# Optimization experiments

Measured on AMD Instinct MI355X. Metric: run time of the kernel, lower is better.

The kernel has to match this reference:

```python
import jax, jax.numpy as jnp
import numpy as np

B, S, D = 1, 1024, 4096
N_HEADS, N_KV, HEAD_DIM = 32, 8, 128
ALPHA = 5.0
BUDGET = 0.2
NEG = -10000.0


def rotate_half(x):
    x1 = x[..., : x.shape[-1] // 2]
    x2 = x[..., x.shape[-1] // 2 :]
    return jnp.concatenate((-x2, x1), axis=-1)


def kv_cache_mask(scores):
    # scores: [b, h, T, S]. Faithful vectorized version of the torch per-row
    # topk/scatter loop (capacity=1.0 => eviction loop body never executes).
    b, h, T, Ssrc = scores.shape
    attn = scores.reshape(b * h, T, Ssrc)
    causal_add = jnp.triu(jnp.full((T, Ssrc), NEG, scores.dtype), 1)
    attn = attn + causal_add
    # torch: torch.max(attn, -1, keepdim=True)[0][0] -> row maxes of head 0 only
    max_val = jnp.max(attn[0], axis=-1, keepdims=True)  # [T, 1]
    fetch_num = jnp.sum(attn >= (max_val - ALPHA), axis=-1)  # [BH, T]
    fetch_num = jnp.mean(fetch_num.astype(scores.dtype), axis=0).astype(jnp.int32)  # [T]
    fetch_max = int(Ssrc * BUDGET)
    fetch_num = jnp.minimum(fetch_num, fetch_max)
    # rank of every column within its (row-causal-masked) row, descending score
    order = jnp.argsort(-attn, axis=-1)           # [BH, T, S]
    ranks = jnp.argsort(order, axis=-1)           # [BH, T, S]
    rows = jnp.arange(T)
    keep_topk = ranks < fetch_num[None, :, None]  # variable-k topk per row
    tril = jnp.arange(Ssrc)[None, :] <= rows[:, None]  # dense causal rows
    fetch = jnp.where((rows < fetch_max)[None, :, None], tril[None], keep_topk)
    mask = jnp.where(fetch, 0.0, NEG).astype(scores.dtype).reshape(b, h, T, Ssrc)
    density = fetch.astype(jnp.float32).sum() / (b * h) / (T * (T + 1) / 2)
    return mask, density


def setup_inputs() -> dict:
    key = jax.random.key(0)
    ks = jax.random.split(key, 5)
    hidden_states = jax.random.normal(ks[0], (B, S, D), jnp.float32)
    # standard RoPE tables, theta=10000
    inv_freq = 1.0 / (10000.0 ** (np.arange(0, HEAD_DIM, 2, dtype=np.float64) / HEAD_DIM))
    freqs = np.outer(np.arange(S, dtype=np.float64), inv_freq)  # [S, hd/2]
    emb = np.concatenate([freqs, freqs], axis=-1)               # [S, hd]
    cos = jnp.asarray(np.cos(emb), jnp.float32)[None]           # [1, S, hd]
    sin = jnp.asarray(np.sin(emb), jnp.float32)[None]
    Wq = jax.random.normal(ks[1], (N_HEADS * HEAD_DIM, D), jnp.float32) * 0.02
    Wk = jax.random.normal(ks[2], (N_KV * HEAD_DIM, D), jnp.float32) * 0.02
    Wv = jax.random.normal(ks[3], (N_KV * HEAD_DIM, D), jnp.float32) * 0.02
    Wo = jax.random.normal(ks[4], (D, N_HEADS * HEAD_DIM), jnp.float32) * 0.02
    return {"hidden_states": hidden_states, "cos": cos, "sin": sin,
            "Wq": Wq, "Wk": Wk, "Wv": Wv, "Wo": Wo}


def reference(hidden_states, cos, sin, Wq, Wk, Wv, Wo):
    b, s, d = hidden_states.shape
    scaling = HEAD_DIM ** -0.5
    q = (hidden_states @ Wq.T).reshape(b, s, N_HEADS, HEAD_DIM).transpose(0, 2, 1, 3)
    k = (hidden_states @ Wk.T).reshape(b, s, N_KV, HEAD_DIM).transpose(0, 2, 1, 3)
    v = (hidden_states @ Wv.T).reshape(b, s, N_KV, HEAD_DIM).transpose(0, 2, 1, 3)
    c = cos[:, None]  # [b, 1, s, hd]
    sn = sin[:, None]
    q = q * c + rotate_half(q) * sn
    k = k * c + rotate_half(k) * sn
    n_rep = N_HEADS // N_KV
    k = jnp.repeat(k, n_rep, axis=1)
    v = jnp.repeat(v, n_rep, axis=1)
    scores = jnp.einsum("bhqd,bhkd->bhqk", q, k) * scaling
    mask, _density = kv_cache_mask(scores)
    probs = jax.nn.softmax(scores + mask, axis=-1)
    out = jnp.einsum("bhqk,bhkd->bhqd", probs, v)
    out = out.transpose(0, 2, 1, 3).reshape(b, s, N_HEADS * HEAD_DIM)
    return out @ Wo.T
```

## Files before the change

### kernel.cpp

```cpp
#include <hip/hip_runtime.h>
#include <hip/hip_bf16.h>
#include <hip/hip_fp16.h>

typedef unsigned int u32;
typedef unsigned short u16;
typedef __bf16 bf16x8 __attribute__((ext_vector_type(8)));
typedef float floatx4 __attribute__((ext_vector_type(4)));

#define SCALE 0.08838834764831845f
#define FETCH_MAX 204

__device__ __forceinline__ float bf2f(u16 u) {
    union { u32 i; float f; } v; v.i = ((u32)u) << 16; return v.f;
}
__device__ __forceinline__ u16 f2bf(float f) {
    union { float f; u32 i; } v; v.f = f;
    u32 r = v.i + 0x7FFFu + ((v.i >> 16) & 1u);
    return (u16)(r >> 16);
}
__device__ __forceinline__ u16 f2h_bits(float f) {
    __half h = __float2half(f);
    union { __half h; u16 u; } v; v.h = h; return v.u;
}
__device__ __forceinline__ float h_bits2f(u16 u) {
    union { __half h; u16 u; } v; v.u = u; return __half2float(v.h);
}
__device__ __forceinline__ u32 h2key(u16 hb) {
    return (u32)(u16)(hb ^ ((hb & 0x8000u) ? 0xFFFFu : 0x8000u));
}
__device__ __forceinline__ u16 key2h(u32 k) {
    return (u16)((k & 0x8000u) ? (k ^ 0x8000u) : (k ^ 0xFFFFu));
}
__device__ __forceinline__ void gld_lds16(const void* g, void* l) {
    __builtin_amdgcn_global_load_lds(
        (const __attribute__((address_space(1))) void*)g,
        (__attribute__((address_space(3))) void*)l, 16, 0, 0);
}

__global__ void detect_k(const u32* cosw, int* flag) {
    if (threadIdx.x == 0 && blockIdx.x == 0)
        *flag = (cosw[0] == 0x3F800000u) ? 1 : 0;
}

__global__ __launch_bounds__(256) void zero_k(int* p, int n) {
    int i = blockIdx.x * 256 + threadIdx.x;
    if (i < n) p[i] = 0;
}

__global__ __launch_bounds__(256) void convert_k(
    const int* flagp, const float* hs, const float* wq, const float* wk,
    const float* wv, const float* wo,
    u16* chs, u16* cwq, u16* cwk, u16* cwv, u16* cwo)
{
    if (*flagp == 0) return;
    const long S0 = 4194304/4, S1 = 16777216/4, S2 = 4194304/4, S3 = 4194304/4, S4 = 16777216/4;
    const long total = S0+S1+S2+S3+S4;
    for (long idx = (long)blockIdx.x*256 + threadIdx.x; idx < total; idx += (long)gridDim.x*256) {
        const float* src; u16* dst; long o = idx;
        if (o < S0)            { src = hs; dst = chs; }
        else if ((o -= S0) < S1) { src = wq; dst = cwq; }
        else if ((o -= S1) < S2) { src = wk; dst = cwk; }
        else if ((o -= S2) < S3) { src = wv; dst = cwv; }
        else                   { o -= S3; src = wo; dst = cwo; }
        float4 v = ((const float4*)src)[o];
        u32 lo = (u32)f2bf(v.x) | ((u32)f2bf(v.y) << 16);
        u32 hi = (u32)f2bf(v.z) | ((u32)f2bf(v.w) << 16);
        ((uint2*)dst)[o] = make_uint2(lo, hi);
    }
}

__global__ __launch_bounds__(256) void gemm_bt(
    const int* flagp,
    const u16* A0, const u16* A1,
    const u16* B0a, const u16* B0b,
    const u16* B1a, const u16* B1b,
    const u16* B2a, const u16* B2b,
    int n0, int n1,
    u16* Cb, float* Cf,
    int M, int N, int K, int ldc)
{
    const int flag = *flagp;
    const u16* A  = flag ? A1 : A0;
    const u16* Bq = flag ? B0b : B0a;
    const u16* Bk = flag ? B1b : B1a;
    const u16* Bv = flag ? B2b : B2a;
    __shared__ u16 Al[128][64];
    __shared__ u16 Bl[128][64];
    const int tid = threadIdx.x;
    const int wave = tid >> 6, lane = tid & 63;
    const int qd = lane >> 4, l16 = lane & 15;
    const int wm = wave & 1, wn = wave >> 1;
    const int m0 = blockIdx.y * 128, nb = blockIdx.x * 128;
    floatx4 acc[4][4];
    floatx4 zf = {0.f, 0.f, 0.f, 0.f};
    for (int mt = 0; mt < 4; ++mt) for (int nt = 0; nt < 4; ++nt) acc[mt][nt] = zf;

    for (int k0 = 0; k0 < K; k0 += 64) {
        #pragma unroll
        for (int it = 0; it < 4; ++it) {
            int idx = tid + it*256;
            int r = idx >> 3, c8 = idx & 7;
            gld_lds16(&A[(size_t)(m0 + r)*K + k0 + c8*8], &Al[r][c8*8]);
            int f = nb + r;
            const u16* Brow = (f < n0) ? (Bq + (size_t)f*K)
                             : (f < n0 + n1) ? (Bk + (size_t)(f - n0)*K)
                             : (Bv + (size_t)(f - n0 - n1)*K);
            gld_lds16(&Brow[k0 + c8*8], &Bl[r][c8*8]);
        }
        __syncthreads();
        #pragma unroll
        for (int ks = 0; ks < 2; ++ks) {
            bf16x8 af[4], bfr[4];
            #pragma unroll
            for (int mt = 0; mt < 4; ++mt)
                af[mt] = *(const bf16x8*)&Al[wm*64 + mt*16 + l16][ks*32 + qd*8];
            #pragma unroll
            for (int nt = 0; nt < 4; ++nt)
                bfr[nt] = *(const bf16x8*)&Bl[wn*64 + nt*16 + l16][ks*32 + qd*8];
            #pragma unroll
            for (int mt = 0; mt < 4; ++mt)
                #pragma unroll
                for (int nt = 0; nt < 4; ++nt)
                    acc[mt][nt] = __builtin_amdgcn_mfma_f32_16x16x32_bf16(af[mt], bfr[nt], acc[mt][nt], 0, 0, 0);
        }
        __syncthreads();
    }
    const bool of32 = (Cf != nullptr) && flag;
    #pragma unroll
    for (int mt = 0; mt < 4; ++mt)
        #pragma unroll
        for (int nt = 0; nt < 4; ++nt)
            #pragma unroll
            for (int rg = 0; rg < 4; ++rg) {
                int row = m0 + wm*64 + mt*16 + qd*4 + rg;
                int col = nb + wn*64 + nt*16 + l16;
                float v = acc[mt][nt][rg];
                if (of32) Cf[(size_t)row*ldc + col] = v;
                else      Cb[(size_t)row*ldc + col] = f2bf(v);
            }
}

__global__ __launch_bounds__(256) void rope_k(const int* flagp, u16* QKV,
                                              const void* cosp, const void* sinp)
{
    const int flag = *flagp;
    long idx = (long)blockIdx.x*256 + threadIdx.x;
    int d = (int)(idx & 63);
    int t = (int)(idx >> 6);
    int slot = t % 40, i = t / 40;
    int col0 = (slot < 32) ? slot*128 : 4096 + (slot - 32)*128;
    size_t base = (size_t)i*6144 + col0;
    float q1 = bf2f(QKV[base + d]), q2 = bf2f(QKV[base + d + 64]);
    float c, s;
    if (flag) { c = ((const float*)cosp)[i*128 + d]; s = ((const float*)sinp)[i*128 + d]; }
    else      { c = bf2f(((const u16*)cosp)[i*128 + d]); s = bf2f(((const u16*)sinp)[i*128 + d]); }
    QKV[base + d]      = f2bf(q1*c - q2*s);
    QKV[base + d + 64] = f2bf(q2*c + q1*s);
}

__global__ __launch_bounds__(256) void vtrans_k(const u16* QKV, u16* VT)
{
    const int b = blockIdx.x;
    const int g = b >> 5, db = (b >> 4) & 1, jb = b & 15;
    __shared__ u16 t[64][72];
    const int tid = threadIdx.x;
    #pragma unroll
    for (int it = 0; it < 2; ++it) {
        int idx = tid + it*256;
        int jj = idx >> 3, c8 = idx & 7;
        uint4 v = *(const uint4*)&QKV[(size_t)(jb*64 + jj)*6144 + 5120 + g*128 + db*64 + c8*8];
        *(uint4*)&t[jj][c8*8] = v;
    }
    __syncthreads();
    #pragma unroll
    for (int it = 0; it < 2; ++it) {
        int idx = tid + it*256;
        int dd = idx >> 3, c8 = idx & 7;
        u16 tmp[8];
        #pragma unroll
        for (int e = 0; e < 8; ++e) tmp[e] = t[c8*8 + e][dd];
        *(uint4*)&VT[(size_t)(g*128 + db*64 + dd)*1024 + jb*64 + c8*8] = *(uint4*)tmp;
    }
}

__global__ __launch_bounds__(256) void rowmax0_k(const u16* QKV, float* rowmax0)
{
    const int i = blockIdx.x;
    __shared__ float Qs[128];
    __shared__ float wm4[4];
    const int tid = threadIdx.x, wave = tid >> 6, lane = tid & 63;
    if (tid < 16) {
        uint4 v = *(const uint4*)&QKV[(size_t)i*6144 + tid*8];
        Qs[tid*8+0] = bf2f((u16)(v.x & 0xffff)); Qs[tid*8+1] = bf2f((u16)(v.x >> 16));
        Qs[tid*8+2] = bf2f((u16)(v.y & 0xffff)); Qs[tid*8+3] = bf2f((u16)(v.y >> 16));
        Qs[tid*8+4] = bf2f((u16)(v.z & 0xffff)); Qs[tid*8+5] = bf2f((u16)(v.z >> 16));
        Qs[tid*8+6] = bf2f((u16)(v.w & 0xffff)); Qs[tid*8+7] = bf2f((u16)(v.w >> 16));
    }
    __syncthreads();
    float mx = -3.0e38f;
    for (int j = tid; j <= i; j += 256) {
        const u16* Kr = &QKV[(size_t)j*6144 + 4096];
        float acc = 0.f;
        #pragma unroll
        for (int c8 = 0; c8 < 16; ++c8) {
            uint4 v = *(const uint4*)&Kr[c8*8];
            acc += Qs[c8*8+0]*bf2f((u16)(v.x & 0xffff)) + Qs[c8*8+1]*bf2f((u16)(v.x >> 16));
            acc += Qs[c8*8+2]*bf2f((u16)(v.y & 0xffff)) + Qs[c8*8+3]*bf2f((u16)(v.y >> 16));
            acc += Qs[c8*8+4]*bf2f((u16)(v.z & 0xffff)) + Qs[c8*8+5]*bf2f((u16)(v.z >> 16));
            acc += Qs[c8*8+6]*bf2f((u16)(v.w & 0xffff)) + Qs[c8*8+7]*bf2f((u16)(v.w >> 16));
        }
        mx = fmaxf(mx, acc * SCALE);
    }
    #pragma unroll
    for (int off = 1; off < 64; off <<= 1) mx = fmaxf(mx, __shfl_xor(mx, off, 64));
    if (lane == 0) wm4[wave] = mx;
    __syncthreads();
    if (tid == 0) rowmax0[i] = fmaxf(fmaxf(wm4[0], wm4[1]), fmaxf(wm4[2], wm4[3]));
}

__global__ __launch_bounds__(256) void score_count(
    const u16* QKV, const float* rowmax0, int* count_sum, u16* Sg)
{
    const int bid = blockIdx.x;
    const int h = bid >> 6, rb = 63 - (bid & 63);
    const int r0 = rb * 16, g = h >> 2;
    const int q4 = rb >> 2, rm4 = rb & 3;
    const int jtc = q4 + 1;
    const int jt64 = jtc * 64;
    const size_t sbase = ((size_t)h*544 + (size_t)jtc*(2*q4 + rm4)) * 1024;
    const int tid = threadIdx.x, wave = tid >> 6, lane = tid & 63;
    const int qd = lane >> 4, l16 = lane & 15;
    __shared__ u16 SP[16][1032];
    __shared__ int redcnt[4][16];

    bf16x8 af[4];
    #pragma unroll
    for (int ks = 0; ks < 4; ++ks)
        af[ks] = *(const bf16x8*)&QKV[(size_t)(r0 + l16)*6144 + h*128 + ks*32 + qd*8];

    float rm0[4]; int runcnt[4];
    #pragma unroll
    for (int rg = 0; rg < 4; ++rg) {
        runcnt[rg] = 0;
        rm0[rg] = rowmax0[r0 + qd*4 + rg] - 5.0f;
    }

    #pragma unroll 2
    for (int ct = 0; ct < jtc; ++ct) {
        const int jc = ct*64 + wave*16 + l16;
        floatx4 sa = {0.f, 0.f, 0.f, 0.f};
        #pragma unroll
        for (int ks = 0; ks < 4; ++ks) {
            bf16x8 bfr = *(const bf16x8*)&QKV[(size_t)jc*6144 + 4096 + g*128 + ks*32 + qd*8];
            sa = __builtin_amdgcn_mfma_f32_16x16x32_bf16(af[ks], bfr, sa, 0, 0, 0);
        }
        #pragma unroll
        for (int rg = 0; rg < 4; ++rg) {
            float s = sa[rg] * SCALE;
            int i = r0 + qd*4 + rg;
            if (jc <= i && s >= rm0[rg]) runcnt[rg]++;
            SP[qd*4 + rg][jc] = f2h_bits(s);
        }
    }
    #pragma unroll
    for (int off = 1; off < 16; off <<= 1)
        #pragma unroll
        for (int rg = 0; rg < 4; ++rg)
            runcnt[rg] += __shfl_xor(runcnt[rg], off, 64);
    if (l16 == 0)
        #pragma unroll
        for (int rg = 0; rg < 4; ++rg)
            redcnt[wave][qd*4 + rg] = runcnt[rg];
    __syncthreads();
    #pragma unroll
    for (int mm = 0; mm < 4; ++mm) {
        const int m = wave*4 + mm;
        for (int c = lane; c < jtc*8; c += 64)
            *(uint4*)&Sg[sbase + (size_t)m*jt64 + c*8] = *(const uint4*)&SP[m][c*8];
    }
    if (tid < 16) {
        int c = redcnt[0][tid] + redcnt[1][tid] + redcnt[2][tid] + redcnt[3][tid];
        atomicAdd(&count_sum[r0 + tid], c);
    }
}

__global__ __launch_bounds__(256, 4) void select_attn(
    const u16* Sg, const u16* VT, const int* count_sum, u16* attn)
{
    const int bid = blockIdx.x;
    const int h = bid >> 6, rb = 63 - (bid & 63);
    const int r0 = rb * 16, g = h >> 2;
    const int q4 = rb >> 2, rm4 = rb & 3;
    const int jtc = q4 + 1;
    const int jt64 = jtc * 64;
    const size_t sbase = ((size_t)h*544 + (size_t)jtc*(2*q4 + rm4)) * 1024;
    const int tid = threadIdx.x, wave = tid >> 6, lane = tid & 63;
    const int qd = lane >> 4, l16 = lane & 15;
    __shared__ u16 SP[16][1032];
    __shared__ float denom[16];

    #pragma unroll
    for (int mm = 0; mm < 4; ++mm) {
        const int m = wave*4 + mm;
        for (int c = lane; c < jtc*8; c += 64)
            *(uint4*)&SP[m][c*8] = *(const uint4*)&Sg[sbase + (size_t)m*jt64 + c*8];
    }
    __syncthreads();

    for (int batch = 0; batch < 4; ++batch) {
        const int m = batch*4 + wave;
        const int i = r0 + m, n = i + 1;
        const bool full = (i < FETCH_MAX);

        u32 key[16];
        #pragma unroll
        for (int c = 0; c < 16; ++c) {
            u32 kk = 0u;
            if (c*64 < n) {
                int j = c*64 + lane;
                u32 t = h2key(SP[m][j]);
                kk = (j < n) ? t : 0u;
            }
            key[c] = kk;
        }

        u32 kmax = key[0];
        #pragma unroll
        for (int c = 1; c < 16; ++c) kmax = (key[c] > kmax) ? key[c] : kmax;
        #pragma unroll
        for (int off = 1; off < 64; off <<= 1) {
            u32 o = (u32)__shfl_xor((int)kmax, off, 64);
            kmax = (o > kmax) ? o : kmax;
        }
        const float rmax = h_bits2f(key2h(kmax));

        u32 Kstar = 0; int quota = 0;
        if (!full) {
            int k = count_sum[i] >> 5;
            if (k > FETCH_MAX) k = FETCH_MAX;
            if (k < 1) k = 1;
            u32 t = 0;
            #pragma unroll 1
            for (int bit = 15; bit >= 0; --bit) {
                u32 tc = t | (1u << bit);
                int cnt = 0;
                #pragma unroll
                for (int c = 0; c < 16; ++c)
                    if (c*64 < n)
                        cnt += __popcll(__ballot(key[c] >= tc));
                if (cnt >= k) t = tc;
            }
            Kstar = t;
            int cntgt = 0;
            #pragma unroll
            for (int c = 0; c < 16; ++c)
                if (c*64 < n)
                    cntgt += __popcll(__ballot(key[c] > Kstar));
            quota = k - cntgt;
        }

        float psum = 0.f; int eqbase = 0;
        #pragma unroll
        for (int c = 0; c < 16; ++c) {
            if (c < jtc) {
                float p = 0.f;
                if (c*64 < n) {
                    int j = c*64 + lane;
                    bool valid = (j < n);
                    bool keep;
                    if (full) keep = valid;
                    else {
                        bool eq = valid && (key[c] == Kstar);
                        unsigned long long em = __ballot(eq);
                        int rk = eqbase + __popcll(em & ((1ull << lane) - 1ull));
                        keep = valid && ((key[c] > Kstar) || (eq && rk < quota));
                        eqbase += __popcll(em);
                    }
                    if (keep) p = __expf(h_bits2f(key2h(key[c])) - rmax);
                }
                psum += p;
                SP[m][c*64 + lane] = f2bf(p);
            }
        }
        #pragma unroll
        for (int off = 1; off < 64; off <<= 1) psum += __shfl_xor(psum, off, 64);
        if (lane == 0) denom[m] = psum;
    }
    __syncthreads();

    floatx4 oacc[2];
    floatx4 zf = {0.f, 0.f, 0.f, 0.f};
    oacc[0] = zf; oacc[1] = zf;
    const u16* VTg = VT + (size_t)g*128*1024;
    #pragma unroll 2
    for (int jt = 0; jt < jtc; ++jt) {
        #pragma unroll
        for (int ks = 0; ks < 2; ++ks) {
            bf16x8 pa = *(const bf16x8*)&SP[l16][jt*64 + ks*32 + qd*8];
            #pragma unroll
            for (int nt = 0; nt < 2; ++nt) {
                bf16x8 bv = *(const bf16x8*)&VTg[(size_t)(wave*32 + nt*16 + l16)*1024 + jt*64 + ks*32 + qd*8];
                oacc[nt] = __builtin_amdgcn_mfma_f32_16x16x32_bf16(pa, bv, oacc[nt], 0, 0, 0);
            }
        }
    }
    #pragma unroll
    for (int nt = 0; nt < 2; ++nt)
        #pragma unroll
        for (int rg = 0; rg < 4; ++rg) {
            int m = qd*4 + rg;
            float v = oacc[nt][rg] / denom[m];
            attn[(size_t)(r0 + m)*4096 + (h << 7) + wave*32 + nt*16 + l16] = f2bf(v);
        }
}

extern "C" void kernel_launch(void* const* d_in, const int* in_sizes, int n_in,
                              void* d_out, int out_size, void* d_ws, size_t ws_size,
                              hipStream_t stream)
{
    const void* hs = d_in[0];
    const void* cs = d_in[1];
    const void* sn = d_in[2];
    const void* wq = d_in[3];
    const void* wk = d_in[4];
    const void* wv = d_in[5];
    const void* wo = d_in[6];
    (void)in_sizes; (void)n_in; (void)out_size; (void)ws_size;

    unsigned char* W = (unsigned char*)d_ws;
    int*    flag  = (int*)   (W);
    int*    cnt   = (int*)   (W + 256);
    float*  rmax0 = (float*) (W + 4608);
    u16*    qkv   = (u16*)   (W + 139776);
    u16*    attn  = (u16*)   (W + 12722688);
    u16*    chs   = (u16*)   (W + 21111296);
    u16*    cwq   = (u16*)   (W + 29499904);
    u16*    cwk   = (u16*)   (W + 63054336);
    u16*    cwv   = (u16*)   (W + 71442944);
    u16*    cwo   = (u16*)   (W + 79831552);
    u16*    vt    = (u16*)   (W + 21111296);
    u16*    scrs  = (u16*)   (W + 29499904);

    detect_k<<<1, 64, 0, stream>>>((const u32*)cs, flag);
    convert_k<<<4096, 256, 0, stream>>>(flag, (const float*)hs, (const float*)wq,
                                        (const float*)wk, (const float*)wv, (const float*)wo,
                                        chs, cwq, cwk, cwv, cwo);
    gemm_bt<<<dim3(48, 8), 256, 0, stream>>>(flag,
        (const u16*)hs, chs,
        (const u16*)wq, cwq, (const u16*)wk, cwk, (const u16*)wv, cwv,
        4096, 1024, qkv, nullptr, 1024, 6144, 4096, 6144);
    vtrans_k<<<256, 256, 0, stream>>>(qkv, vt);
    rope_k<<<10240, 256, 0, stream>>>(flag, qkv, cs, sn);
    rowmax0_k<<<1024, 256, 0, stream>>>(qkv, rmax0);
    zero_k<<<4, 256, 0, stream>>>(cnt, 1024);
    score_count<<<2048, 256, 0, stream>>>(qkv, rmax0, cnt, scrs);
    select_attn<<<2048, 256, 0, stream>>>(scrs, vt, cnt, attn);
    gemm_bt<<<dim3(32, 8), 256, 0, stream>>>(flag,
        attn, attn,
        (const u16*)wo, cwo, (const u16*)wo, cwo, (const u16*)wo, cwo,
        4096, 4096, (u16*)d_out, (float*)d_out, 1024, 4096, 4096, 4096);
}
```

Baseline: 604.6 us.

## Pair long and short row blocks per select_attn block and swizzle GEMM LDS

The select_attn kernel now handles two row blocks per workgroup: one long causal block paired with one short block, so every workgroup gets a balanced amount of work. The second block's scores are loaded asynchronously into a second LDS buffer while the first block's top-k selection runs, and the count values are prefetched into registers. Separately, the GEMM's LDS tiles use an XOR swizzle on 16-byte columns to cut bank conflicts on the MFMA fragment reads. The cost is double the LDS per block (about 66KB) with occupancy lowered to 2 blocks per CU, and half as many workgroups.

```diff
diff --git a/kernel.cpp b/kernel.cpp
--- a/kernel.cpp
+++ b/kernel.cpp
@@ -100,12 +100,13 @@
         for (int it = 0; it < 4; ++it) {
             int idx = tid + it*256;
             int r = idx >> 3, c8 = idx & 7;
-            gld_lds16(&A[(size_t)(m0 + r)*K + k0 + c8*8], &Al[r][c8*8]);
+            int c8s = c8 ^ (r & 7);
+            gld_lds16(&A[(size_t)(m0 + r)*K + k0 + c8s*8], &Al[r][c8*8]);
             int f = nb + r;
             const u16* Brow = (f < n0) ? (Bq + (size_t)f*K)
                              : (f < n0 + n1) ? (Bk + (size_t)(f - n0)*K)
                              : (Bv + (size_t)(f - n0 - n1)*K);
-            gld_lds16(&Brow[k0 + c8*8], &Bl[r][c8*8]);
+            gld_lds16(&Brow[k0 + c8s*8], &Bl[r][c8*8]);
         }
         __syncthreads();
         #pragma unroll
@@ -113,10 +114,10 @@
             bf16x8 af[4], bfr[4];
             #pragma unroll
             for (int mt = 0; mt < 4; ++mt)
-                af[mt] = *(const bf16x8*)&Al[wm*64 + mt*16 + l16][ks*32 + qd*8];
+                af[mt] = *(const bf16x8*)&Al[wm*64 + mt*16 + l16][((ks*4 + qd) ^ (l16 & 7))*8];
             #pragma unroll
             for (int nt = 0; nt < 4; ++nt)
-                bfr[nt] = *(const bf16x8*)&Bl[wn*64 + nt*16 + l16][ks*32 + qd*8];
+                bfr[nt] = *(const bf16x8*)&Bl[wn*64 + nt*16 + l16][((ks*4 + qd) ^ (l16 & 7))*8];
             #pragma unroll
             for (int mt = 0; mt < 4; ++mt)
                 #pragma unroll
@@ -284,29 +285,11 @@
     }
 }
 
-__global__ __launch_bounds__(256, 4) void select_attn(
-    const u16* Sg, const u16* VT, const int* count_sum, u16* attn)
-{
-    const int bid = blockIdx.x;
-    const int h = bid >> 6, rb = 63 - (bid & 63);
-    const int r0 = rb * 16, g = h >> 2;
-    const int q4 = rb >> 2, rm4 = rb & 3;
-    const int jtc = q4 + 1;
-    const int jt64 = jtc * 64;
-    const size_t sbase = ((size_t)h*544 + (size_t)jtc*(2*q4 + rm4)) * 1024;
-    const int tid = threadIdx.x, wave = tid >> 6, lane = tid & 63;
-    const int qd = lane >> 4, l16 = lane & 15;
-    __shared__ u16 SP[16][1032];
-    __shared__ float denom[16];
-
-    #pragma unroll
-    for (int mm = 0; mm < 4; ++mm) {
-        const int m = wave*4 + mm;
-        for (int c = lane; c < jtc*8; c += 64)
-            *(uint4*)&SP[m][c*8] = *(const uint4*)&Sg[sbase + (size_t)m*jt64 + c*8];
-    }
-    __syncthreads();
-
+__device__ __forceinline__ void phase_b(u16 (*SPt)[1032], float* denomt,
+                                        const int* kc, int r0, int jtc,
+                                        int wave, int lane)
+{
+    #pragma unroll
     for (int batch = 0; batch < 4; ++batch) {
         const int m = batch*4 + wave;
         const int i = r0 + m, n = i + 1;
@@ -318,7 +301,7 @@
             u32 kk = 0u;
             if (c*64 < n) {
                 int j = c*64 + lane;
-                u32 t = h2key(SP[m][j]);
+                u32 t = h2key(SPt[m][j]);
                 kk = (j < n) ? t : 0u;
             }
             key[c] = kk;
@@ -336,7 +319,7 @@
 
         u32 Kstar = 0; int quota = 0;
         if (!full) {
-            int k = count_sum[i] >> 5;
+            int k = kc[batch] >> 5;
             if (k > FETCH_MAX) k = FETCH_MAX;
             if (k < 1) k = 1;
             u32 t = 0;
@@ -379,24 +362,28 @@
                     if (keep) p = __expf(h_bits2f(key2h(key[c])) - rmax);
                 }
                 psum += p;
-                SP[m][c*64 + lane] = f2bf(p);
+                SPt[m][c*64 + lane] = f2bf(p);
             }
         }
         #pragma unroll
         for (int off = 1; off < 64; off <<= 1) psum += __shfl_xor(psum, off, 64);
-        if (lane == 0) denom[m] = psum;
-    }
-    __syncthreads();
-
+        if (lane == 0) denomt[m] = psum;
+    }
+}
+
+__device__ __forceinline__ void phase_c(const u16 (*SPt)[1032], const float* denomt,
+                                        const u16* VTg, u16* attn, int r0, int jtc,
+                                        int h, int wave, int lane)
+{
+    const int qd = lane >> 4, l16 = lane & 15;
     floatx4 oacc[2];
     floatx4 zf = {0.f, 0.f, 0.f, 0.f};
     oacc[0] = zf; oacc[1] = zf;
-    const u16* VTg = VT + (size_t)g*128*1024;
     #pragma unroll 2
     for (int jt = 0; jt < jtc; ++jt) {
         #pragma unroll
         for (int ks = 0; ks < 2; ++ks) {
-            bf16x8 pa = *(const bf16x8*)&SP[l16][jt*64 + ks*32 + qd*8];
+            bf16x8 pa = *(const bf16x8*)&SPt[l16][jt*64 + ks*32 + qd*8];
             #pragma unroll
             for (int nt = 0; nt < 2; ++nt) {
                 bf16x8 bv = *(const bf16x8*)&VTg[(size_t)(wave*32 + nt*16 + l16)*1024 + jt*64 + ks*32 + qd*8];
@@ -409,9 +396,58 @@
         #pragma unroll
         for (int rg = 0; rg < 4; ++rg) {
             int m = qd*4 + rg;
-            float v = oacc[nt][rg] / denom[m];
+            float v = oacc[nt][rg] / denomt[m];
             attn[(size_t)(r0 + m)*4096 + (h << 7) + wave*32 + nt*16 + l16] = f2bf(v);
         }
+}
+
+__global__ __launch_bounds__(256, 2) void select_attn(
+    const u16* Sg, const u16* VT, const int* count_sum, u16* attn)
+{
+    const int b = blockIdx.x;
+    const int h = b >> 5, p = b & 31, g = h >> 2;
+    const int rb0 = 63 - p, rb1 = p;
+    const int q40 = rb0 >> 2, jtc0 = q40 + 1, r00 = rb0 * 16;
+    const int q41 = rb1 >> 2, jtc1 = q41 + 1, r01 = rb1 * 16;
+    const size_t sb0 = ((size_t)h*544 + (size_t)jtc0*(2*q40 + (rb0 & 3))) * 1024;
+    const size_t sb1 = ((size_t)h*544 + (size_t)jtc1*(2*q41 + (rb1 & 3))) * 1024;
+    const int tid = threadIdx.x, wave = tid >> 6, lane = tid & 63;
+    __shared__ u16 SP[2][16][1032];
+    __shared__ float denom[2][16];
+    const u16* VTg = VT + (size_t)g*128*1024;
+
+    #pragma unroll
+    for (int mm = 0; mm < 4; ++mm) {
+        const int m = wave*4 + mm;
+        for (int c = lane; c < jtc0*8; c += 64)
+            gld_lds16(&Sg[sb0 + (size_t)m*(jtc0*64) + (size_t)c*8], &SP[0][m][c*8]);
+    }
+    int kc0[4], kc1[4];
+    #pragma unroll
+    for (int bb = 0; bb < 4; ++bb) {
+        kc0[bb] = count_sum[r00 + bb*4 + wave];
+        kc1[bb] = count_sum[r01 + bb*4 + wave];
+    }
+    #pragma unroll
+    for (int bb = 0; bb < 4; ++bb)
+        asm volatile("" : "+v"(kc0[bb]), "+v"(kc1[bb]));
+    __syncthreads();
+
+    #pragma unroll
+    for (int mm = 0; mm < 4; ++mm) {
+        const int m = wave*4 + mm;
+        for (int c = lane; c < jtc1*8; c += 64)
+            gld_lds16(&Sg[sb1 + (size_t)m*(jtc1*64) + (size_t)c*8], &SP[1][m][c*8]);
+    }
+
+    phase_b(SP[0], denom[0], kc0, r00, jtc0, wave, lane);
+    __syncthreads();
+
+    phase_c(SP[0], denom[0], VTg, attn, r00, jtc0, h, wave, lane);
+    phase_b(SP[1], denom[1], kc1, r01, jtc1, wave, lane);
+    __syncthreads();
+
+    phase_c(SP[1], denom[1], VTg, attn, r01, jtc1, h, wave, lane);
 }
 
 extern "C" void kernel_launch(void* const* d_in, const int* in_sizes, int n_in,
@@ -454,7 +490,7 @@
     rowmax0_k<<<1024, 256, 0, stream>>>(qkv, rmax0);
     zero_k<<<4, 256, 0, stream>>>(cnt, 1024);
     score_count<<<2048, 256, 0, stream>>>(qkv, rmax0, cnt, scrs);
-    select_attn<<<2048, 256, 0, stream>>>(scrs, vt, cnt, attn);
+    select_attn<<<1024, 256, 0, stream>>>(scrs, vt, cnt, attn);
     gemm_bt<<<dim3(32, 8), 256, 0, stream>>>(flag,
         attn, attn,
         (const u16*)wo, cwo, (const u16*)wo, cwo, (const u16*)wo, cwo,
```

After: 571.0 us. 1.06x faster.
